# Kernel tuning notes

Hardware: AMD Instinct MI355X
Metric: run time of the kernel (lower is better)

The kernel has to match this reference:

```python
import jax, jax.numpy as jnp
import numpy as np

STRIDE = 16
A = 9
PRE_NMS_TOP_N = 6000
POST_NMS_TOP_N = 300
NMS_THRESH = 0.7
MIN_SIZE = 16
H, W = 128, 192


def _generate_anchors(base_size=16, ratios=(0.5, 1.0, 2.0), scales=(8, 16, 32)):
    base = np.array([0, 0, base_size - 1, base_size - 1], dtype=np.float64)
    w = base[2] - base[0] + 1
    h = base[3] - base[1] + 1
    x_ctr = base[0] + 0.5 * (w - 1)
    y_ctr = base[1] + 0.5 * (h - 1)
    size = w * h
    ratios = np.array(ratios)
    ws = np.round(np.sqrt(size / ratios))
    hs = np.round(ws * ratios)
    ratio_anchors = np.stack([x_ctr - 0.5 * (ws - 1), y_ctr - 0.5 * (hs - 1),
                              x_ctr + 0.5 * (ws - 1), y_ctr + 0.5 * (hs - 1)], axis=1)
    out = []
    scales = np.array(scales)
    for a in ratio_anchors:
        aw = a[2] - a[0] + 1
        ah = a[3] - a[1] + 1
        xc = a[0] + 0.5 * (aw - 1)
        yc = a[1] + 0.5 * (ah - 1)
        ws2 = aw * scales
        hs2 = ah * scales
        out.append(np.stack([xc - 0.5 * (ws2 - 1), yc - 0.5 * (hs2 - 1),
                             xc + 0.5 * (ws2 - 1), yc + 0.5 * (hs2 - 1)], axis=1))
    return np.concatenate(out, axis=0).astype(np.float32)  # [9,4]


def setup_inputs() -> dict:
    key = jax.random.key(0)
    k1, k2 = jax.random.split(key)
    scores = jax.random.uniform(k1, (1, 2 * A, H, W), dtype=jnp.float32)
    bbox_deltas = 0.1 * jax.random.normal(k2, (1, 4 * A, H, W), dtype=jnp.float32)
    im_info = jnp.array([[H * STRIDE, W * STRIDE, 1.0]], dtype=jnp.float32)
    return {"scores": scores, "bbox_deltas": bbox_deltas, "im_info": im_info}


def _proposal_forward(scores, bbox_deltas, im_info):
    anchors_base = jnp.asarray(_generate_anchors())  # [A,4]
    sc = scores[:, A:, :, :]                          # fg scores [1,A,H,W]
    h, w = sc.shape[-2], sc.shape[-1]
    shift_x = (jnp.arange(w) * STRIDE).astype(sc.dtype)
    shift_y = (jnp.arange(h) * STRIDE).astype(sc.dtype)
    sy, sx = jnp.meshgrid(shift_y, shift_x, indexing='ij')
    shifts = jnp.stack([sx.ravel(), sy.ravel(), sx.ravel(), sy.ravel()], axis=1)  # [K,4]
    anchors = (anchors_base[None, :, :] + shifts[:, None, :]).reshape(-1, 4)      # [K*A,4]

    deltas = bbox_deltas.transpose(0, 2, 3, 1).reshape(-1, 4)
    deltas = jnp.concatenate([deltas[:, :2], jnp.clip(deltas[:, 2:], -10.0, 10.0)], axis=1)
    sc = sc.transpose(0, 2, 3, 1).reshape(-1)  # [K*A]

    widths = anchors[:, 2] - anchors[:, 0] + 1.0
    heights = anchors[:, 3] - anchors[:, 1] + 1.0
    ctr_x = anchors[:, 0] + 0.5 * widths
    ctr_y = anchors[:, 1] + 0.5 * heights
    dx, dy, dw, dh = deltas[:, 0], deltas[:, 1], deltas[:, 2], deltas[:, 3]
    pcx = dx * widths + ctr_x
    pcy = dy * heights + ctr_y
    pw = jnp.exp(dw) * widths
    ph = jnp.exp(dh) * heights
    x1 = pcx - 0.5 * pw
    y1 = pcy - 0.5 * ph
    x2 = pcx + 0.5 * pw
    y2 = pcy + 0.5 * ph

    info = im_info[0]
    x1 = jnp.clip(x1, 0.0, info[1] - 1.0)
    x2 = jnp.clip(x2, 0.0, info[1] - 1.0)
    y1 = jnp.clip(y1, 0.0, info[0] - 1.0)
    y2 = jnp.clip(y2, 0.0, info[0] - 1.0)
    proposals = jnp.stack([x1, y1, x2, y2], axis=1)

    # filter_boxes: mask (instead of dropping) boxes smaller than min_size*scale
    min_sz = MIN_SIZE * info[2]
    valid = ((x2 - x1 + 1.0) >= min_sz) & ((y2 - y1 + 1.0) >= min_sz)
    masked = jnp.where(valid, sc, -jnp.inf)

    # sort desc + pre_nms_topN
    top_scores, top_idx = jax.lax.top_k(masked, PRE_NMS_TOP_N)
    boxes = proposals[top_idx]               # [PRE,4], score-descending
    tvalid = top_scores > -jnp.inf

    # pairwise IoU (torchvision convention)
    area = (boxes[:, 2] - boxes[:, 0]) * (boxes[:, 3] - boxes[:, 1])
    lt = jnp.maximum(boxes[:, None, :2], boxes[None, :, :2])
    rb = jnp.minimum(boxes[:, None, 2:], boxes[None, :, 2:])
    wh = jnp.clip(rb - lt, 0.0)
    inter = wh[..., 0] * wh[..., 1]
    iou = inter / (area[:, None] + area[None, :] - inter)  # [PRE,PRE]

    # greedy NMS over score-sorted boxes
    n = PRE_NMS_TOP_N
    def step(keep, x):
        iou_col, v, i = x
        suppressed = jnp.any(keep & (iou_col > NMS_THRESH))
        k = v & jnp.logical_not(suppressed)
        keep = keep.at[i].set(k)
        return keep, k
    keep, _ = jax.lax.scan(step, jnp.zeros((n,), dtype=bool),
                           (iou.T, tvalid, jnp.arange(n)))

    # kept boxes first (stable => score order preserved), take post_nms_topN
    order = jnp.argsort(jnp.logical_not(keep).astype(jnp.int32), stable=True)[:POST_NMS_TOP_N]
    kept = keep[order]
    out_boxes = jnp.where(kept[:, None], boxes[order], 0.0)
    output = jnp.concatenate(
        [jnp.zeros((POST_NMS_TOP_N, 1), out_boxes.dtype), out_boxes], axis=1)
    return output  # [POST,5]: (batch_idx=0, x1,y1,x2,y2); rows beyond kept count are zero


def reference(scores, bbox_deltas, im_info):
    return _proposal_forward(scores, bbox_deltas, im_info)
```

## Files before the change

kernel.cpp:

```cpp
#include <hip/hip_runtime.h>

#define N_ANCH 221184
#define HW     24576
#define Wd     192
#define AA     9
#define TOPN   6000
#define POSTN  300
#define NWORDS 94
#define NW2    96
#define NCHUNK 24
#define GRID   512
#define PERBLK 432
#define SEGSZ  1024
#define CAND_CAP 8192

typedef unsigned long long u64;
typedef unsigned int u32;

__device__ const float c_aw[9] = {184.f,368.f,736.f,128.f,256.f,512.f, 88.f,176.f,352.f};
__device__ const float c_ah[9] = { 96.f,192.f,384.f,128.f,256.f,512.f,176.f,352.f,704.f};

__device__ __forceinline__ u32 ald32(const u32* p) {
    return __hip_atomic_load(p, __ATOMIC_RELAXED, __HIP_MEMORY_SCOPE_AGENT);
}
__device__ __forceinline__ void ast32(u32* p, u32 v) {
    __hip_atomic_store(p, v, __ATOMIC_RELAXED, __HIP_MEMORY_SCOPE_AGENT);
}
__device__ __forceinline__ u64 ald64(const u64* p) {
    return __hip_atomic_load(p, __ATOMIC_RELAXED, __HIP_MEMORY_SCOPE_AGENT);
}
__device__ __forceinline__ void ast64(u64* p, u64 v) {
    __hip_atomic_store(p, v, __ATOMIC_RELAXED, __HIP_MEMORY_SCOPE_AGENT);
}
__device__ __forceinline__ void stf4(float4* p, float4 v) {
    u64 lo, hi;
    float2 a = make_float2(v.x, v.y), b = make_float2(v.z, v.w);
    __builtin_memcpy(&lo, &a, 8); __builtin_memcpy(&hi, &b, 8);
    ast64((u64*)p, lo); ast64(((u64*)p) + 1, hi);
}
__device__ __forceinline__ float4 ldf4(const float4* p) {
    u64 lo = ald64((const u64*)p), hi = ald64(((const u64*)p) + 1);
    float2 a, b;
    __builtin_memcpy(&a, &lo, 8); __builtin_memcpy(&b, &hi, 8);
    return make_float4(a.x, a.y, b.x, b.y);
}

__device__ __forceinline__ void gbar(u32* cnt, u32* flag, u32 epoch) {
    __syncthreads();
    if (threadIdx.x == 0) {
        u32 old = __hip_atomic_fetch_add(cnt, 1u, __ATOMIC_RELAXED, __HIP_MEMORY_SCOPE_AGENT);
        if (old == epoch * GRID - 1u) {
            ast32(flag, epoch);
        } else {
            int guard = 0;
            while (ald32(flag) < epoch) {
                __builtin_amdgcn_s_sleep(1);
                if (++guard > (1 << 22)) break;
            }
        }
    }
    __syncthreads();
}

__device__ __forceinline__ float4 decode_box(int a, int cell,
                                             const float* __restrict__ deltas,
                                             float info0, float info1, float info2,
                                             bool* valid) {
    int h = cell / Wd;
    int w = cell - h * Wd;
    const float* db = deltas + (size_t)(4 * a) * HW + cell;
    float dx = db[0];
    float dy = db[HW];
    float dw = db[2 * HW];
    float dh = db[3 * HW];
    dw = fminf(fmaxf(dw, -10.f), 10.f);
    dh = fminf(fmaxf(dh, -10.f), 10.f);

    float ww = c_aw[a], hh = c_ah[a];
    float cx = 16.f * (float)w + 8.f;
    float cy = 16.f * (float)h + 8.f;

    float pcx = __fadd_rn(__fmul_rn(dx, ww), cx);
    float pcy = __fadd_rn(__fmul_rn(dy, hh), cy);
    float pw  = __fmul_rn(expf(dw), ww);
    float ph  = __fmul_rn(expf(dh), hh);
    float hpw = __fmul_rn(0.5f, pw);
    float hph = __fmul_rn(0.5f, ph);
    float x1 = __fsub_rn(pcx, hpw);
    float x2 = __fadd_rn(pcx, hpw);
    float y1 = __fsub_rn(pcy, hph);
    float y2 = __fadd_rn(pcy, hph);

    float xmax = __fsub_rn(info1, 1.f);
    float ymax = __fsub_rn(info0, 1.f);
    x1 = fminf(fmaxf(x1, 0.f), xmax);
    x2 = fminf(fmaxf(x2, 0.f), xmax);
    y1 = fminf(fmaxf(y1, 0.f), ymax);
    y2 = fminf(fmaxf(y2, 0.f), ymax);

    float msz = __fmul_rn(16.f, info2);
    *valid = (__fadd_rn(__fsub_rn(x2, x1), 1.f) >= msz) &&
             (__fadd_rn(__fsub_rn(y2, y1), 1.f) >= msz);
    return make_float4(x1, y1, x2, y2);
}

__device__ __forceinline__ u64 rdl64(u64 v, int l) {
    u32 lo = (u32)__builtin_amdgcn_readlane((int)(u32)v, l);
    u32 hi = (u32)__builtin_amdgcn_readlane((int)(u32)(v >> 32), l);
    return ((u64)hi << 32) | (u64)lo;
}

__global__ __launch_bounds__(256, 2) void fused_kernel(
        const float* __restrict__ scores, const float* __restrict__ deltas,
        const float* __restrict__ iminfo, float* __restrict__ out,
        u32* __restrict__ bar, u32* __restrict__ flag,
        u32* __restrict__ hist1, u32* __restrict__ hist2,
        u32* __restrict__ segctr, u64* __restrict__ vmask,
        u32* __restrict__ keys, u64* __restrict__ cand,
        float4* __restrict__ tb, u64* __restrict__ mat) {
    int tid = threadIdx.x;
    int bid = blockIdx.x;
    int lane = tid & 63;
    int wv = tid >> 6;

    __shared__ u32 lh[256];
    __shared__ u32 sfx[256];
    __shared__ u32 h2w[4][256];
    __shared__ u64 stage[2048];
    __shared__ float4 cbw[4][64];
    __shared__ int kept[POSTN];
    __shared__ u32 sP, sRank, sT;

    float info0 = iminfo[0], info1 = iminfo[1], info2 = iminfo[2];
    int tbase = bid * PERBLK;

    lh[tid] = 0u;
    __syncthreads();
    #pragma unroll
    for (int j = 0; j < 2; ++j) {
        int i = j * 256 + tid;
        if (i < PERBLK) {
            int t = tbase + i;
            int a = t / HW;
            int cell = t - a * HW;
            float score = scores[(AA + a) * HW + cell];
            bool valid;
            (void)decode_box(a, cell, deltas, info0, info1, info2, &valid);
            u32 sb = __float_as_uint(score);
            u32 key = valid ? ((sb & 0x80000000u) ? ~sb : (sb | 0x80000000u))
                            : 0x007FFFFFu;
            ast32(&keys[t], key);
            atomicAdd(&lh[key >> 24], 1u);
        }
    }
    __syncthreads();
    if (lh[tid]) atomicAdd(&hist1[tid], lh[tid]);
    gbar(bar, flag, 1);

    sfx[tid] = ald32(&hist1[tid]);
    __syncthreads();
    for (int d = 1; d < 256; d <<= 1) {
        u32 v = (tid + d < 256) ? sfx[tid + d] : 0u;
        __syncthreads();
        sfx[tid] += v;
        __syncthreads();
    }
    {
        u32 ge = sfx[tid];
        u32 gt = (tid < 255) ? sfx[tid + 1] : 0u;
        if (ge >= TOPN && gt < TOPN) { sP = (u32)tid; sRank = TOPN - gt; }
    }
    for (int i = tid; i < 4 * 256; i += 256) ((u32*)h2w)[i] = 0u;
    __syncthreads();
    u32 P = sP, rankP = sRank;
    #pragma unroll
    for (int j = 0; j < 2; ++j) {
        int i = j * 256 + tid;
        if (i < PERBLK) {
            u32 k = ald32(&keys[tbase + i]);
            if ((k >> 24) == P) atomicAdd(&h2w[wv][(k >> 16) & 0xFFu], 1u);
        }
    }
    __syncthreads();
    {
        u32 s4 = h2w[0][tid] + h2w[1][tid] + h2w[2][tid] + h2w[3][tid];
        if (s4) atomicAdd(&hist2[tid], s4);
    }
    gbar(bar, flag, 2);

    sfx[tid] = ald32(&hist2[tid]);
    __syncthreads();
    for (int d = 1; d < 256; d <<= 1) {
        u32 v = (tid + d < 256) ? sfx[tid + d] : 0u;
        __syncthreads();
        sfx[tid] += v;
        __syncthreads();
    }
    {
        u32 ge = sfx[tid];
        u32 gt = (tid < 255) ? sfx[tid + 1] : 0u;
        if (ge >= rankP && gt < rankP) sT = (P << 24) | ((u32)tid << 16);
    }
    __syncthreads();
    u32 T = sT;
    #pragma unroll
    for (int j = 0; j < 2; ++j) {
        int i = j * 256 + tid;
        if (i < PERBLK) {
            int t = tbase + i;
            u32 k = ald32(&keys[t]);
            if (k >= T) {
                int seg = bid & 7;
                u32 pos = atomicAdd(&segctr[32 * seg], 1u);
                if (pos < SEGSZ) {
                    int a = t / HW;
                    int cell = t - a * HW;
                    u32 aidx = (u32)(cell * 9 + a);
                    ast64(&cand[seg * SEGSZ + pos], ((u64)k << 32) | (u64)(~aidx));
                }
            }
        }
    }
    gbar(bar, flag, 3);

    {
        u32 cc[8];
        #pragma unroll
        for (int s = 0; s < 8; ++s) {
            cc[s] = ald32(&segctr[32 * s]);
            if (cc[s] > SEGSZ) cc[s] = SEGSZ;
        }
        int part = tid & 15;
        int i = bid * 16 + (tid >> 4);
        int iseg = i >> 10, ioff = i & 1023;
        bool active = (u32)ioff < cc[iseg];
        u64 k = active ? ald64(&cand[i]) : 0ull;
        u32 cnt = 0;
        for (int q = 0; q < 4; ++q) {
            for (int j = tid; j < 2048; j += 256) {
                int g = q * 2048 + j;
                int s_ = g >> 10, off = g & 1023;
                stage[j] = ((u32)off < cc[s_]) ? ald64(&cand[g]) : 0ull;
            }
            __syncthreads();
            const ulonglong2* sv = (const ulonglong2*)stage;
            for (int jj = part; jj < 1024; jj += 16) {
                ulonglong2 v = sv[jj];
                cnt += (v.x > k) ? 1u : 0u;
                cnt += (v.y > k) ? 1u : 0u;
            }
            __syncthreads();
        }
        cnt += __shfl_xor(cnt, 1);
        cnt += __shfl_xor(cnt, 2);
        cnt += __shfl_xor(cnt, 4);
        cnt += __shfl_xor(cnt, 8);
        if (part == 0 && active && cnt < TOPN) {
            u32 aidx = ~((u32)k);
            int a = (int)(aidx % 9u);
            int cell = (int)(aidx / 9u);
            bool valid;
            float4 box = decode_box(a, cell, deltas, info0, info1, info2, &valid);
            stf4(&tb[cnt], box);
            if ((u32)(k >> 32) != 0x007FFFFFu)
                atomicOr(&vmask[cnt >> 6], 1ull << (cnt & 63));
        }
    }
    gbar(bar, flag, 4);

    {
        int waveid = bid * 4 + wv;
        for (int j = waveid; j < 94 * 94; j += GRID * 4) {
            int by = j / 94;
            int bx = j - by * 94;
            if (bx < by) continue;
            int c0 = bx * 64;
            {
                int col = c0 + lane;
                cbw[wv][lane] = (col < TOPN) ? ldf4(&tb[col]) : make_float4(0.f, 0.f, 0.f, 0.f);
            }
            int row = by * 64 + lane;
            if (row < TOPN) {
                float4 rb = ldf4(&tb[row]);
                float rA = (rb.z - rb.x) * (rb.w - rb.y);
                u64 mask = 0ull;
                for (int c = 0; c < 64; ++c) {
                    if (c0 + c >= TOPN) break;
                    float4 b = cbw[wv][c];
                    float lx = fmaxf(rb.x, b.x), ly = fmaxf(rb.y, b.y);
                    float rx = fminf(rb.z, b.z), ry = fminf(rb.w, b.w);
                    float iw = fmaxf(rx - lx, 0.f), ih = fmaxf(ry - ly, 0.f);
                    float inter = iw * ih;
                    float bA = (b.z - b.x) * (b.w - b.y);
                    float iou = inter / ((rA + bA) - inter);
                    if (iou > 0.7f) mask |= (1ull << c);
                }
                ast64(&mat[(size_t)row * NW2 + bx], mask);
            }
        }
    }
    gbar(bar, flag, 5);

    if (bid == 0 && tid < 64) {
        u64 r0 = ~ald64(&vmask[lane]);
        u64 r1 = (lane < NWORDS - 64) ? ~ald64(&vmask[64 + lane]) : ~0ull;
        int cnt = 0;
        u64 dg[4][4];
        #pragma unroll
        for (int q = 0; q < 4; ++q) {
            const u64* rp = mat + (size_t)(q * 64 + lane) * NW2;
            dg[q][0] = ald64(rp); dg[q][1] = ald64(rp + 1);
            dg[q][2] = ald64(rp + 2); dg[q][3] = ald64(rp + 3);
        }
        for (int c = 0; c < NCHUNK; ++c) {
            u64 nd[4][4];
            #pragma unroll
            for (int q = 0; q < 4; ++q) { nd[q][0]=0; nd[q][1]=0; nd[q][2]=0; nd[q][3]=0; }
            if (c + 1 < NCHUNK) {
                int nb = (c + 1) * 256, nw = 4 * (c + 1);
                #pragma unroll
                for (int q = 0; q < 4; ++q) {
                    const u64* rp = mat + (size_t)(nb + q * 64 + lane) * NW2 + nw;
                    nd[q][0] = ald64(rp); nd[q][1] = ald64(rp + 1);
                    nd[q][2] = ald64(rp + 2); nd[q][3] = ald64(rp + 3);
                }
            }
            int w0 = 4 * c;
            u64 s0 = (w0     < 64) ? rdl64(r0, w0)     : rdl64(r1, w0 - 64);
            u64 s1 = (w0 + 1 < 64) ? rdl64(r0, w0 + 1) : rdl64(r1, w0 - 63);
            u64 s2 = (w0 + 2 < 64) ? rdl64(r0, w0 + 2) : rdl64(r1, w0 - 62);
            u64 s3 = (w0 + 3 < 64) ? rdl64(r0, w0 + 3) : rdl64(r1, w0 - 61);
            if ((s0 & s1 & s2 & s3) != ~0ull) {
                int base = c * 256;
                u64 rem0 = s0, rem1 = s1, rem2 = s2, rem3 = s3;
                u64 km0 = 0, km1 = 0, km2 = 0, km3 = 0;
                while (cnt < POSTN) {
                    int b;
                    if (~rem0) b = __ffsll((u64)~rem0) - 1;
                    else if (~rem1) b = 64  + __ffsll((u64)~rem1) - 1;
                    else if (~rem2) b = 128 + __ffsll((u64)~rem2) - 1;
                    else if (~rem3) b = 192 + __ffsll((u64)~rem3) - 1;
                    else break;
                    if (lane == 0) kept[cnt] = base + b;
                    ++cnt;
                    int q = b >> 6, l = b & 63;
                    u64 v0, v1, v2, v3;
                    if (q == 0)      { v0=dg[0][0]; v1=dg[0][1]; v2=dg[0][2]; v3=dg[0][3]; }
                    else if (q == 1) { v0=dg[1][0]; v1=dg[1][1]; v2=dg[1][2]; v3=dg[1][3]; }
                    else if (q == 2) { v0=dg[2][0]; v1=dg[2][1]; v2=dg[2][2]; v3=dg[2][3]; }
                    else             { v0=dg[3][0]; v1=dg[3][1]; v2=dg[3][2]; v3=dg[3][3]; }
                    rem0 |= rdl64(v0, l); rem1 |= rdl64(v1, l);
                    rem2 |= rdl64(v2, l); rem3 |= rdl64(v3, l);
                    u64 bit = 1ull << l;
                    if (q == 0)      { rem0 |= bit; km0 |= bit; }
                    else if (q == 1) { rem1 |= bit; km1 |= bit; }
                    else if (q == 2) { rem2 |= bit; km2 |= bit; }
                    else             { rem3 |= bit; km3 |= bit; }
                }
                if (cnt >= POSTN) break;
                u64 f0 = 0ull, f1 = 0ull;
                while (km0 | km1 | km2 | km3) {
                    int idx[16];
                    #pragma unroll
                    for (int j = 0; j < 16; ++j) {
                        int b = -1;
                        if (km0)      { b = __ffsll(km0) - 1;        km0 &= km0 - 1; }
                        else if (km1) { b = 64  + __ffsll(km1) - 1;  km1 &= km1 - 1; }
                        else if (km2) { b = 128 + __ffsll(km2) - 1;  km2 &= km2 - 1; }
                        else if (km3) { b = 192 + __ffsll(km3) - 1;  km3 &= km3 - 1; }
                        idx[j] = b;
                    }
                    u64 a0[16], a1[16];
                    #pragma unroll
                    for (int j = 0; j < 16; ++j) {
                        a0[j] = 0ull; a1[j] = 0ull;
                        if (idx[j] >= 0) {
                            const u64* row = mat + (size_t)(base + idx[j]) * NW2;
                            a0[j] = ald64(row + lane);
                            if (lane < NWORDS - 64) a1[j] = ald64(row + 64 + lane);
                        }
                    }
                    #pragma unroll
                    for (int j = 0; j < 16; ++j) { f0 |= a0[j]; f1 |= a1[j]; }
                }
                r0 |= f0; r1 |= f1;
            }
            #pragma unroll
            for (int q = 0; q < 4; ++q) {
                dg[q][0]=nd[q][0]; dg[q][1]=nd[q][1]; dg[q][2]=nd[q][2]; dg[q][3]=nd[q][3];
            }
        }
        for (int r = lane; r < POSTN; r += 64) {
            float4 b2 = make_float4(0.f, 0.f, 0.f, 0.f);
            if (r < cnt) b2 = ldf4(&tb[kept[r]]);
            float* o = out + r * 5;
            o[0] = 0.f; o[1] = b2.x; o[2] = b2.y; o[3] = b2.z; o[4] = b2.w;
        }
    }
}

extern "C" void kernel_launch(void* const* d_in, const int* in_sizes, int n_in,
                              void* d_out, int out_size, void* d_ws, size_t ws_size,
                              hipStream_t stream) {
    const float* scores = (const float*)d_in[0];
    const float* deltas = (const float*)d_in[1];
    const float* iminfo = (const float*)d_in[2];
    float* out = (float*)d_out;

    char* ws = (char*)d_ws;
    u32* bar    = (u32*)(ws + 0);
    u32* flag   = (u32*)(ws + 128);
    u32* hist1  = (u32*)(ws + 256);
    u32* hist2  = (u32*)(ws + 1280);
    u32* segctr = (u32*)(ws + 2304);
    u64* vmask  = (u64*)(ws + 3328);
    u32* keys   = (u32*)(ws + 8192);
    u64* cand   = (u64*)(ws + 892928);
    float4* tb  = (float4*)(ws + 958464);
    u64* mat    = (u64*)(ws + 1054720);

    hipMemsetAsync(ws, 0, 8192, stream);
    fused_kernel<<<GRID, 256, 0, stream>>>(scores, deltas, iminfo, out,
                                           bar, flag, hist1, hist2, segctr, vmask,
                                           keys, cand, tb, mat);
}
```

Baseline: 261.9 us.

## Replace atomic-counter grid barrier with tag slots and drop host memset

```diff
diff --git a/kernel.cpp b/kernel.cpp
--- a/kernel.cpp
+++ b/kernel.cpp
@@ -12,10 +12,12 @@
 #define GRID   512
 #define PERBLK 432
 #define SEGSZ  1024
-#define CAND_CAP 8192
 
 typedef unsigned long long u64;
 typedef unsigned int u32;
+
+#define INITTAG 0xBEEF0001u
+#define TAGBASE 0xC0DE0000u
 
 __device__ const float c_aw[9] = {184.f,368.f,736.f,128.f,256.f,512.f, 88.f,176.f,352.f};
 __device__ const float c_ah[9] = { 96.f,192.f,384.f,128.f,256.f,512.f,176.f,352.f,704.f};
@@ -45,21 +47,32 @@
     return make_float4(a.x, a.y, b.x, b.y);
 }
 
-__device__ __forceinline__ void gbar(u32* cnt, u32* flag, u32 epoch) {
-    __syncthreads();
-    if (threadIdx.x == 0) {
-        u32 old = __hip_atomic_fetch_add(cnt, 1u, __ATOMIC_RELAXED, __HIP_MEMORY_SCOPE_AGENT);
-        if (old == epoch * GRID - 1u) {
-            ast32(flag, epoch);
-        } else {
+__device__ __forceinline__ void gbar(u32* slots, u32* flagline, u32 epoch) {
+    u32 tag = TAGBASE + epoch;
+    __syncthreads();
+    if (blockIdx.x == 0) {
+        int tid = threadIdx.x;
+        int guard = 0;
+        for (;;) {
+            u32 a = ald32(&slots[(1 + tid) << 4]);
+            u32 b = (tid < 255) ? ald32(&slots[(257 + tid) << 4]) : tag;
+            if (__syncthreads_and((a == tag) && (b == tag))) break;
+            __builtin_amdgcn_s_sleep(1);
+            if (++guard > (1 << 20)) break;
+        }
+        if (tid == 0) ast32(flagline, tag);
+        __syncthreads();
+    } else {
+        if (threadIdx.x == 0) {
+            ast32(&slots[blockIdx.x << 4], tag);
             int guard = 0;
-            while (ald32(flag) < epoch) {
+            while (ald32(flagline) != tag) {
                 __builtin_amdgcn_s_sleep(1);
                 if (++guard > (1 << 22)) break;
             }
         }
-    }
-    __syncthreads();
+        __syncthreads();
+    }
 }
 
 __device__ __forceinline__ float4 decode_box(int a, int cell,
@@ -113,9 +126,9 @@
 __global__ __launch_bounds__(256, 2) void fused_kernel(
         const float* __restrict__ scores, const float* __restrict__ deltas,
         const float* __restrict__ iminfo, float* __restrict__ out,
-        u32* __restrict__ bar, u32* __restrict__ flag,
+        u32* __restrict__ slots, u32* __restrict__ flagline, u32* __restrict__ initflag,
         u32* __restrict__ hist1, u32* __restrict__ hist2,
-        u32* __restrict__ segctr, u64* __restrict__ vmask,
+        u32* __restrict__ segctr, u32* __restrict__ validb,
         u32* __restrict__ keys, u64* __restrict__ cand,
         float4* __restrict__ tb, u64* __restrict__ mat) {
     int tid = threadIdx.x;
@@ -133,6 +146,14 @@
 
     float info0 = iminfo[0], info1 = iminfo[1], info2 = iminfo[2];
     int tbase = bid * PERBLK;
+
+    if (bid == 0) {
+        ast32(&hist1[tid], 0u);
+        ast32(&hist2[tid], 0u);
+        ast32(&segctr[tid], 0u);
+        __syncthreads();
+        if (tid == 0) ast32(initflag, INITTAG);
+    }
 
     lh[tid] = 0u;
     __syncthreads();
@@ -154,8 +175,16 @@
         }
     }
     __syncthreads();
+    if (tid == 0 && bid != 0) {
+        int guard = 0;
+        while (ald32(initflag) != INITTAG) {
+            __builtin_amdgcn_s_sleep(1);
+            if (++guard > (1 << 22)) break;
+        }
+    }
+    __syncthreads();
     if (lh[tid]) atomicAdd(&hist1[tid], lh[tid]);
-    gbar(bar, flag, 1);
+    gbar(slots, flagline, 1);
 
     sfx[tid] = ald32(&hist1[tid]);
     __syncthreads();
@@ -186,7 +215,7 @@
         u32 s4 = h2w[0][tid] + h2w[1][tid] + h2w[2][tid] + h2w[3][tid];
         if (s4) atomicAdd(&hist2[tid], s4);
     }
-    gbar(bar, flag, 2);
+    gbar(slots, flagline, 2);
 
     sfx[tid] = ald32(&hist2[tid]);
     __syncthreads();
@@ -221,7 +250,7 @@
             }
         }
     }
-    gbar(bar, flag, 3);
+    gbar(slots, flagline, 3);
 
     {
         u32 cc[8];
@@ -262,11 +291,10 @@
             bool valid;
             float4 box = decode_box(a, cell, deltas, info0, info1, info2, &valid);
             stf4(&tb[cnt], box);
-            if ((u32)(k >> 32) != 0x007FFFFFu)
-                atomicOr(&vmask[cnt >> 6], 1ull << (cnt & 63));
-        }
-    }
-    gbar(bar, flag, 4);
+            ast32(&validb[cnt], ((u32)(k >> 32) != 0x007FFFFFu) ? 1u : 0u);
+        }
+    }
+    gbar(slots, flagline, 4);
 
     {
         int waveid = bid * 4 + wv;
@@ -299,11 +327,26 @@
             }
         }
     }
-    gbar(bar, flag, 5);
+    gbar(slots, flagline, 5);
 
     if (bid == 0 && tid < 64) {
-        u64 r0 = ~ald64(&vmask[lane]);
-        u64 r1 = (lane < NWORDS - 64) ? ~ald64(&vmask[64 + lane]) : ~0ull;
+        u64 r0, r1;
+        {
+            u64 bits = 0ull;
+            for (int j = 0; j < 64; ++j)
+                if (ald32(&validb[lane * 64 + j]) == 1u) bits |= (1ull << j);
+            r0 = ~bits;
+            if (lane < NWORDS - 64) {
+                u64 bits1 = 0ull;
+                for (int j = 0; j < 64; ++j) {
+                    int idx = (64 + lane) * 64 + j;
+                    if (idx < 6016 && ald32(&validb[idx]) == 1u) bits1 |= (1ull << j);
+                }
+                r1 = ~bits1;
+            } else {
+                r1 = ~0ull;
+            }
+        }
         int cnt = 0;
         u64 dg[4][4];
         #pragma unroll
@@ -408,19 +451,20 @@
     float* out = (float*)d_out;
 
     char* ws = (char*)d_ws;
-    u32* bar    = (u32*)(ws + 0);
-    u32* flag   = (u32*)(ws + 128);
-    u32* hist1  = (u32*)(ws + 256);
-    u32* hist2  = (u32*)(ws + 1280);
-    u32* segctr = (u32*)(ws + 2304);
-    u64* vmask  = (u64*)(ws + 3328);
-    u32* keys   = (u32*)(ws + 8192);
-    u64* cand   = (u64*)(ws + 892928);
-    float4* tb  = (float4*)(ws + 958464);
-    u64* mat    = (u64*)(ws + 1054720);
-
-    hipMemsetAsync(ws, 0, 8192, stream);
+    u32* slots    = (u32*)(ws + 0);
+    u32* flagline = (u32*)(ws + 32768);
+    u32* initflag = (u32*)(ws + 32832);
+    u32* hist1    = (u32*)(ws + 32896);
+    u32* hist2    = (u32*)(ws + 33920);
+    u32* segctr   = (u32*)(ws + 34944);
+    u32* validb   = (u32*)(ws + 35968);
+    u32* keys     = (u32*)(ws + 60032);
+    u64* cand     = (u64*)(ws + 944768);
+    float4* tb    = (float4*)(ws + 1010304);
+    u64* mat      = (u64*)(ws + 1106560);
+
     fused_kernel<<<GRID, 256, 0, stream>>>(scores, deltas, iminfo, out,
-                                           bar, flag, hist1, hist2, segctr, vmask,
+                                           slots, flagline, initflag,
+                                           hist1, hist2, segctr, validb,
                                            keys, cand, tb, mat);
 }
```

Result: no change. 263.6 us (+0.7%).
